# Kernel optimization log

Hardware: AMD Instinct MI355X
Metric: run time of the kernel (lower is better)

## Reference

```python
import jax, jax.numpy as jnp
import numpy as np

N = 50000      # number of nodes (src == dst, homogeneous block)
E = 800000     # number of edges
H = 2          # num_heads
D = 32         # out_dim per head
IN = 64        # target input feature dim
DMID = 64      # 'mid' node-type feature dim
EREL = 200000  # size of 'rel' edge feature table
DREL = 32      # 'rel' edge feature dim
ED = 2 * D     # edge_dim (concat of mid + rel virtual feats per head)


def setup_inputs() -> dict:
    key = jax.random.key(0)
    ks = jax.random.split(key, 18)
    s = 0.05
    return {
        "h": jax.random.normal(ks[0], (N, IN), jnp.float32),
        "W_t": jax.random.normal(ks[1], (IN, H * D), jnp.float32) * s,
        "b_t": jax.random.normal(ks[2], (H * D,), jnp.float32) * s,
        "nfeat_mid": jax.random.normal(ks[3], (N, DMID), jnp.float32),
        "W_mid": jax.random.normal(ks[4], (DMID, H * D), jnp.float32) * s,
        "b_mid": jax.random.normal(ks[5], (H * D,), jnp.float32) * s,
        "efeat_rel": jax.random.normal(ks[6], (EREL, DREL), jnp.float32),
        "W_rel": jax.random.normal(ks[7], (DREL, H * D), jnp.float32) * s,
        "b_rel": jax.random.normal(ks[8], (H * D,), jnp.float32) * s,
        "attn_src": jax.random.normal(ks[9], (1, H, D), jnp.float32) * s,
        "attn_dst": jax.random.normal(ks[10], (1, H, D), jnp.float32) * s,
        "attn_edge": jax.random.normal(ks[11], (1, H, ED), jnp.float32) * s,
        "W_edge": jax.random.normal(ks[12], (ED, D), jnp.float32) * s,
        "b_edge": jax.random.normal(ks[13], (D,), jnp.float32) * s,
        "src_idx": jax.random.randint(ks[14], (E,), 0, N, jnp.int32),
        "dst_idx": jax.random.randint(ks[15], (E,), 0, N, jnp.int32),
        "hn": jax.random.randint(ks[16], (E, 1), 0, N, jnp.int32),
        "he": jax.random.randint(ks[17], (E, 1), 0, EREL, jnp.int32),
    }


def reference(h, W_t, b_t, nfeat_mid, W_mid, b_mid, efeat_rel, W_rel, b_rel,
              attn_src, attn_dst, attn_edge, W_edge, b_edge,
              src_idx, dst_idx, hn, he):
    # target node projection -> [N, H, D]
    hp = (h @ W_t + b_t).reshape(-1, H, D)
    # per-node attention logits (GAT style) -> [N, H]
    e_src = jnp.sum(attn_src * jax.nn.relu(hp), axis=-1)
    e_dst = jnp.sum(attn_dst * jax.nn.relu(hp), axis=-1)
    # per-edge logits: u_add_v -> [E, H]
    e = e_src[src_idx] + e_dst[dst_idx]

    # virtual edge features gathered along metapath: [E, H, 2D]
    hn_f = (nfeat_mid @ W_mid + b_mid).reshape(-1, H, D)[hn[:, 0]]
    he_f = (efeat_rel @ W_rel + b_rel).reshape(-1, H, D)[he[:, 0]]
    h_e = jnp.concatenate([hn_f, he_f], axis=-1)
    e = e + jnp.sum(attn_edge * jax.nn.relu(h_e), axis=-1)

    # edge_softmax: segment softmax over incoming edges of each dst node
    m = jax.ops.segment_max(e, dst_idx, num_segments=N)
    m = jnp.where(jnp.isfinite(m), m, 0.0)  # zero-degree nodes
    ex = jnp.exp(e - m[dst_idx])
    denom = jax.ops.segment_sum(ex, dst_idx, num_segments=N)
    a = ex / denom[dst_idx]                  # [E, H]

    # u_mul_e scatter-sum aggregation -> [N, H, D]
    rst = jax.ops.segment_sum(hp[src_idx] * a[..., None], dst_idx, num_segments=N)
    # edge-feature aggregation -> [N, H, 2D], then fc_edge
    ft2 = jax.ops.segment_sum(h_e * a[..., None], dst_idx, num_segments=N)
    rst = rst + ft2 @ W_edge + b_edge

    # residual + activation
    rst = jax.nn.relu(rst + hp)
    out = rst.reshape(N, H * D)
    # l2 normalize (F.normalize, eps=1e-12)
    out = out / jnp.maximum(jnp.linalg.norm(out, axis=1, keepdims=True), 1e-12)
    return out
```

## Files before the change

### kernel.cpp

```cpp
#include <hip/hip_runtime.h>

typedef unsigned int uint;
#define LOG2E 1.4426950408889634f

__device__ __forceinline__ float bf16_lo(uint v) { return __uint_as_float(v << 16); }
__device__ __forceinline__ float bf16_hi(uint v) { return __uint_as_float(v & 0xffff0000u); }
__device__ __forceinline__ unsigned short f2bf(float f) {
    uint u = __float_as_uint(f);
    return (unsigned short)((u + 0x7fffu + ((u >> 16) & 1u)) >> 16);
}
__device__ __forceinline__ float bf16u(unsigned short s) {
    return __uint_as_float(((uint)s) << 16);
}

template<int K>
__device__ __forceinline__ void proj_body(
    int blk, const float* __restrict__ X, const float* __restrict__ W,
    const float* __restrict__ bias, const float* __restrict__ avec0,
    const float* __restrict__ avec1, int mode, int nrows,
    float* __restrict__ outF32, unsigned short* __restrict__ outF16,
    float2* __restrict__ outA0, float2* __restrict__ outA1,
    float* Xsh, float* Wsh, float* av0sh, float* av1sh, float* bsh)
{
    constexpr int XP = 68;
    int t = threadIdx.x;

    const float4* W4 = (const float4*)W;
    float4* Wsh4 = (float4*)Wsh;
    for (int i = t; i < K * 16; i += 256) Wsh4[i] = W4[i];

    if (t < 64) {
        int head = t >> 5, d = t & 31;
        int aidx = (mode == 0) ? t : (mode == 1 ? head * 64 + d : head * 64 + 32 + d);
        av0sh[t] = avec0 ? avec0[aidx] : 0.f;
        av1sh[t] = avec1 ? avec1[aidx] : 0.f;
        bsh[t] = bias[t];
    }

    int base = blk * 64;
    const float4* X4 = (const float4*)X;
    for (int i = t; i < 64 * (K / 4); i += 256) {
        int row = i / (K / 4), c4 = i % (K / 4);
        int gr = base + row; if (gr >= nrows) gr = nrows - 1;
        *(float4*)&Xsh[row * XP + c4 * 4] = X4[(size_t)gr * (K / 4) + c4];
    }
    __syncthreads();

    int rquad = t >> 4, cq = t & 15;
    float acc[4][4];
#pragma unroll
    for (int ri = 0; ri < 4; ++ri)
#pragma unroll
        for (int ci = 0; ci < 4; ++ci) acc[ri][ci] = 0.f;

#pragma unroll 4
    for (int kq = 0; kq < K / 4; ++kq) {
        float4 wq0 = Wsh4[(4 * kq + 0) * 16 + cq];
        float4 wq1 = Wsh4[(4 * kq + 1) * 16 + cq];
        float4 wq2 = Wsh4[(4 * kq + 2) * 16 + cq];
        float4 wq3 = Wsh4[(4 * kq + 3) * 16 + cq];
#pragma unroll
        for (int ri = 0; ri < 4; ++ri) {
            float4 xq = *(const float4*)&Xsh[(4 * rquad + ri) * XP + 4 * kq];
            acc[ri][0] += xq.x * wq0.x + xq.y * wq1.x + xq.z * wq2.x + xq.w * wq3.x;
            acc[ri][1] += xq.x * wq0.y + xq.y * wq1.y + xq.z * wq2.y + xq.w * wq3.y;
            acc[ri][2] += xq.x * wq0.z + xq.y * wq1.z + xq.z * wq2.z + xq.w * wq3.z;
            acc[ri][3] += xq.x * wq0.w + xq.y * wq1.w + xq.z * wq2.w + xq.w * wq3.w;
        }
    }

    int c0 = cq * 4;
    float4 bv  = *(float4*)&bsh[c0];
    float4 a0v = *(float4*)&av0sh[c0];
    float4 a1v = *(float4*)&av1sh[c0];
    float4 vv[4];
    float s0[4], s1[4];
#pragma unroll
    for (int ri = 0; ri < 4; ++ri) {
        float4 val;
        val.x = acc[ri][0] + bv.x;
        val.y = acc[ri][1] + bv.y;
        val.z = acc[ri][2] + bv.z;
        val.w = acc[ri][3] + bv.w;
        vv[ri] = val;
        float r0 = fmaxf(val.x, 0.f), r1 = fmaxf(val.y, 0.f);
        float r2 = fmaxf(val.z, 0.f), r3 = fmaxf(val.w, 0.f);
        s0[ri] = r0 * a0v.x + r1 * a0v.y + r2 * a0v.z + r3 * a0v.w;
        s1[ri] = r0 * a1v.x + r1 * a1v.y + r2 * a1v.z + r3 * a1v.w;
    }
#pragma unroll
    for (int ri = 0; ri < 4; ++ri) {
        s0[ri] += __shfl_xor(s0[ri], 1, 64);
        s0[ri] += __shfl_xor(s0[ri], 2, 64);
        s0[ri] += __shfl_xor(s0[ri], 4, 64);
        s1[ri] += __shfl_xor(s1[ri], 1, 64);
        s1[ri] += __shfl_xor(s1[ri], 2, 64);
        s1[ri] += __shfl_xor(s1[ri], 4, 64);
    }
    float s0x[4], s1x[4];
#pragma unroll
    for (int ri = 0; ri < 4; ++ri) {
        s0x[ri] = __shfl_xor(s0[ri], 8, 64);
        s1x[ri] = __shfl_xor(s1[ri], 8, 64);
    }

    int rbase = base + rquad * 4;
#pragma unroll
    for (int ri = 0; ri < 4; ++ri) {
        int row = rbase + ri;
        if (row >= nrows) continue;
        if (outF32)
            *(float4*)&outF32[(size_t)row * 64 + c0] = vv[ri];
        uint u0 = (uint)f2bf(vv[ri].x) | ((uint)f2bf(vv[ri].y) << 16);
        uint u1 = (uint)f2bf(vv[ri].z) | ((uint)f2bf(vv[ri].w) << 16);
        *(uint2*)&outF16[(size_t)row * 64 + c0] = make_uint2(u0, u1);
        if (cq == 0 && outA0)
            outA0[row] = make_float2(s0[ri] * LOG2E, s0x[ri] * LOG2E);
        if (cq == 1 && outA1)
            outA1[row] = make_float2(s1[ri] * LOG2E, s1x[ri] * LOG2E);
    }
}

__global__ __launch_bounds__(256) void mega_kernel(
    const float* __restrict__ h, const float* __restrict__ W_t, const float* __restrict__ b_t,
    const float* __restrict__ nfeat_mid, const float* __restrict__ W_mid, const float* __restrict__ b_mid,
    const float* __restrict__ efeat_rel, const float* __restrict__ W_rel, const float* __restrict__ b_rel,
    const float* __restrict__ attn_src, const float* __restrict__ attn_dst, const float* __restrict__ attn_edge,
    const int* __restrict__ dst_idx, int* __restrict__ deg,
    float* __restrict__ hp32, unsigned short* __restrict__ hp16,
    unsigned short* __restrict__ mid16, unsigned short* __restrict__ rel16,
    float2* __restrict__ e_src, float2* __restrict__ e_dst,
    float2* __restrict__ em, float2* __restrict__ er,
    int N, int EREL, int E, int nC, int nA, int nB)
{
    __shared__ float Xsh[64 * 68];
    __shared__ float Wsh[64 * 64];
    __shared__ float av0sh[64], av1sh[64], bsh[64];
    int b = blockIdx.x;
    if (b < nC) {
        proj_body<32>(b, efeat_rel, W_rel, b_rel, attn_edge, nullptr, 2, EREL,
                      nullptr, rel16, er, nullptr, Xsh, Wsh, av0sh, av1sh, bsh);
    } else if (b < nC + nA) {
        proj_body<64>(b - nC, h, W_t, b_t, attn_src, attn_dst, 0, N,
                      hp32, hp16, e_src, e_dst, Xsh, Wsh, av0sh, av1sh, bsh);
    } else if (b < nC + nA + nB) {
        proj_body<64>(b - nC - nA, nfeat_mid, W_mid, b_mid, attn_edge, nullptr, 1, N,
                      nullptr, mid16, em, nullptr, Xsh, Wsh, av0sh, av1sh, bsh);
    } else {
        int i = (b - nC - nA - nB) * 256 + threadIdx.x;
        if (i < E) atomicAdd(&deg[dst_idx[i]], 1);
    }
}

__global__ __launch_bounds__(256) void scanA_kernel(
    const int* __restrict__ deg, int* __restrict__ blkSums, int N)
{
    __shared__ int red[256];
    int t = threadIdx.x;
    int base = blockIdx.x * 1024 + t * 4;
    int s = 0;
    if (base + 3 < N) {
        int4 v = *(const int4*)&deg[base];
        s = v.x + v.y + v.z + v.w;
    } else {
        for (int i = 0; i < 4; ++i) if (base + i < N) s += deg[base + i];
    }
    red[t] = s;
    __syncthreads();
    for (int off = 128; off >= 1; off >>= 1) {
        if (t < off) red[t] += red[t + off];
        __syncthreads();
    }
    if (t == 0) blkSums[blockIdx.x] = red[0];
}

__global__ __launch_bounds__(256) void scanC_kernel(
    const int* __restrict__ deg, const int* __restrict__ blkSums,
    int* __restrict__ row_ptr, int* __restrict__ cursor, int N, int nblk)
{
    __shared__ int sh[256];
    __shared__ int blkOffSh;
    int t = threadIdx.x;
    int blk = blockIdx.x;
    int base = blk * 1024 + t * 4;

    if (t < 64) {
        int s = 0;
        for (int j = t; j < blk; j += 64) s += blkSums[j];
        for (int m = 32; m >= 1; m >>= 1) s += __shfl_xor(s, m, 64);
        if (t == 0) blkOffSh = s;
    }

    int4 v = make_int4(0, 0, 0, 0);
    if (base + 3 < N) v = *(const int4*)&deg[base];
    else {
        if (base < N)     v.x = deg[base];
        if (base + 1 < N) v.y = deg[base + 1];
        if (base + 2 < N) v.z = deg[base + 2];
    }
    int ts = v.x + v.y + v.z + v.w;
    sh[t] = ts;
    __syncthreads();
    for (int off = 1; off < 256; off <<= 1) {
        int val = (t >= off) ? sh[t - off] : 0;
        __syncthreads();
        sh[t] += val;
        __syncthreads();
    }
    int blkOff = blkOffSh;
    int ex = blkOff + ((t == 0) ? 0 : sh[t - 1]);
    int p0 = ex, p1 = ex + v.x, p2 = p1 + v.y, p3 = p2 + v.z;
    if (base < N)     { row_ptr[base]     = p0; cursor[base]     = p0; }
    if (base + 1 < N) { row_ptr[base + 1] = p1; cursor[base + 1] = p1; }
    if (base + 2 < N) { row_ptr[base + 2] = p2; cursor[base + 2] = p2; }
    if (base + 3 < N) { row_ptr[base + 3] = p3; cursor[base + 3] = p3; }
    if (blk == nblk - 1 && t == 255) row_ptr[N] = blkOff + sh[255];
}

__global__ __launch_bounds__(256) void scatter_kernel(
    const int* __restrict__ src, const int* __restrict__ dst,
    const int* __restrict__ hn, const int* __restrict__ he,
    const float2* __restrict__ es, const float2* __restrict__ ed,
    const float2* __restrict__ em, const float2* __restrict__ er,
    int* __restrict__ cursor, uint4* __restrict__ erec, int E)
{
    int i = blockIdx.x * blockDim.x + threadIdx.x;
    if (i >= E) return;
    int s = src[i], d = dst[i], a = hn[i], b = he[i];
    float2 v1 = es[s], v2 = ed[d], v3 = em[a], v4 = er[b];
    float e0 = fminf(fmaxf(v1.x + v2.x + v3.x + v4.x, -60.f), 60.f);
    float e1 = fminf(fmaxf(v1.y + v2.y + v3.y + v4.y, -60.f), 60.f);
    int pos = atomicAdd(&cursor[d], 1);
    erec[pos] = make_uint4((uint)s | ((uint)a << 16), (uint)b,
                           __float_as_uint(e0), __float_as_uint(e1));
}

__global__ __launch_bounds__(256) void aggregate_kernel(
    const int* __restrict__ row_ptr, const uint4* __restrict__ erec,
    const float* __restrict__ hp32,
    const unsigned short* __restrict__ hp16,
    const unsigned short* __restrict__ mid16,
    const unsigned short* __restrict__ rel16,
    const float* __restrict__ We, const float* __restrict__ be,
    float* __restrict__ out, int N)
{
    __shared__ float WeSh[64 * 32];
    __shared__ float ft2sh[4][128];
    int t = threadIdx.x;
    for (int i = t; i < 64 * 32; i += 256) WeSh[i] = We[i];
    __syncthreads();

    int wave = t >> 6, lane = t & 63;
    int head = lane >> 5, dj = lane & 31;
    int n = blockIdx.x * 4 + wave;
    bool valid = n < N;
    int nn = valid ? n : 0;

    int start = row_ptr[nn], end = row_ptr[nn + 1];

    bool isrel = lane >= 32;
    int l31 = lane & 31;
    bool h1w = ((lane >> 4) & 1) != 0;
    const uint* tab32 = (const uint*)(isrel ? rel16 : mid16);
    float rstc = 0.f, fx = 0.f, fy = 0.f, den0 = 0.f, den1 = 0.f;
#pragma unroll 4
    for (int i = start; i < end; ++i) {
        uint4 r = erec[i];
        uint sidx = r.x & 0xffffu;
        float a0 = __builtin_amdgcn_exp2f(__uint_as_float(r.z));
        float a1 = __builtin_amdgcn_exp2f(__uint_as_float(r.w));
        den0 += a0; den1 += a1;
        rstc += bf16u(hp16[(sidx << 6) | (uint)lane]) * (head ? a1 : a0);
        uint ridx = isrel ? r.y : (r.x >> 16);
        uint pv = tab32[(ridx << 5) | (uint)l31];
        float w = h1w ? a1 : a0;
        fx += bf16_lo(pv) * w;
        fy += bf16_hi(pv) * w;
    }
    float inv0 = den0 > 0.f ? 1.f / den0 : 0.f;
    float inv1 = den1 > 0.f ? 1.f / den1 : 0.f;
    rstc *= head ? inv1 : inv0;
    float invf = h1w ? inv1 : inv0;

    int slotbase;
    if (lane < 16)      slotbase = 2 * lane;
    else if (lane < 32) slotbase = 2 * lane + 32;
    else if (lane < 48) slotbase = 2 * lane - 32;
    else                slotbase = 2 * lane;
    ft2sh[wave][slotbase]     = fx * invf;
    ft2sh[wave][slotbase + 1] = fy * invf;

    __builtin_amdgcn_sched_barrier(0);
    asm volatile("s_waitcnt lgkmcnt(0)" ::: "memory");
    __builtin_amdgcn_sched_barrier(0);

    float fc = be[dj];
#pragma unroll 8
    for (int dd = 0; dd < 64; ++dd)
        fc += ft2sh[wave][head * 64 + dd] * WeSh[dd * 32 + dj];

    float val = rstc + fc + hp32[(uint)nn * 64 + lane];
    val = fmaxf(val, 0.f);

    float ss = val * val;
    for (int m = 32; m >= 1; m >>= 1) ss += __shfl_xor(ss, m, 64);
    float invn = 1.f / fmaxf(sqrtf(ss), 1e-12f);
    if (valid) out[(uint)nn * 64 + lane] = val * invn;
}

extern "C" void kernel_launch(void* const* d_in, const int* in_sizes, int n_in,
                              void* d_out, int out_size, void* d_ws, size_t ws_size,
                              hipStream_t stream)
{
    const float* h         = (const float*)d_in[0];
    const float* W_t       = (const float*)d_in[1];
    const float* b_t       = (const float*)d_in[2];
    const float* nfeat_mid = (const float*)d_in[3];
    const float* W_mid     = (const float*)d_in[4];
    const float* b_mid     = (const float*)d_in[5];
    const float* efeat_rel = (const float*)d_in[6];
    const float* W_rel     = (const float*)d_in[7];
    const float* b_rel     = (const float*)d_in[8];
    const float* attn_src  = (const float*)d_in[9];
    const float* attn_dst  = (const float*)d_in[10];
    const float* attn_edge = (const float*)d_in[11];
    const float* W_edge    = (const float*)d_in[12];
    const float* b_edge    = (const float*)d_in[13];
    const int* src_idx     = (const int*)d_in[14];
    const int* dst_idx     = (const int*)d_in[15];
    const int* hn          = (const int*)d_in[16];
    const int* he          = (const int*)d_in[17];
    float* out = (float*)d_out;

    const int N    = in_sizes[0] / 64;
    const int EREL = in_sizes[6] / 32;
    const int E    = in_sizes[14];

    char* ws = (char*)d_ws;
    auto alloc = [&](size_t bytes) {
        void* p = (void*)ws;
        ws += (bytes + 255) & ~(size_t)255;
        return p;
    };
    float* hp32           = (float*)alloc((size_t)N * 64 * 4);
    unsigned short* hp16  = (unsigned short*)alloc((size_t)N * 64 * 2);
    unsigned short* mid16 = (unsigned short*)alloc((size_t)N * 64 * 2);
    unsigned short* rel16 = (unsigned short*)alloc((size_t)EREL * 64 * 2);
    float2* e_src  = (float2*)alloc((size_t)N * 8);
    float2* e_dst  = (float2*)alloc((size_t)N * 8);
    float2* em     = (float2*)alloc((size_t)N * 8);
    float2* er     = (float2*)alloc((size_t)EREL * 8);
    int* deg       = (int*)alloc((size_t)N * 4);
    int* row_ptr   = (int*)alloc((size_t)(N + 1) * 4);
    int* cursor    = (int*)alloc((size_t)N * 4);
    int* blkSums   = (int*)alloc((size_t)64 * 4);
    uint4* erec    = (uint4*)alloc((size_t)E * 16);

    hipMemsetAsync(deg, 0, (size_t)N * 4, stream);

    int nA = (N + 63) / 64;
    int nB = nA;
    int nC = (EREL + 63) / 64;
    int nD = (E + 255) / 256;
    mega_kernel<<<nC + nA + nB + nD, 256, 0, stream>>>(
        h, W_t, b_t, nfeat_mid, W_mid, b_mid, efeat_rel, W_rel, b_rel,
        attn_src, attn_dst, attn_edge, dst_idx, deg,
        hp32, hp16, mid16, rel16, e_src, e_dst, em, er,
        N, EREL, E, nC, nA, nB);

    int nblk = (N + 1023) / 1024;
    scanA_kernel<<<nblk, 256, 0, stream>>>(deg, blkSums, N);
    scanC_kernel<<<nblk, 256, 0, stream>>>(deg, blkSums, row_ptr, cursor, N, nblk);

    scatter_kernel<<<(E + 255) / 256, 256, 0, stream>>>(
        src_idx, dst_idx, hn, he, e_src, e_dst, em, er, cursor, erec, E);

    aggregate_kernel<<<(N + 3) / 4, 256, 0, stream>>>(
        row_ptr, erec, hp32, hp16, mid16, rel16, W_edge, b_edge, out, N);
}
```

Measured before the change: 294.5 us.

## Software-pipeline edge gathers in aggregation and read projection weights from global

The aggregation loop now prefetches the next edge record and its dependent hp16 and table gathers one iteration ahead, so the dependent load chain overlaps with the current edge's arithmetic instead of being serialized. The unroll-by-4 pragma is dropped in favour of this explicit one-deep pipeline. Separately, the projection kernel no longer stages W in shared memory and reads it directly from global/cache, which cuts LDS use (possibly raising occupancy) but adds global loads inside the inner loop.

```diff
diff --git a/kernel.cpp b/kernel.cpp
--- a/kernel.cpp
+++ b/kernel.cpp
@@ -9,8 +9,8 @@
     uint u = __float_as_uint(f);
     return (unsigned short)((u + 0x7fffu + ((u >> 16) & 1u)) >> 16);
 }
-__device__ __forceinline__ float bf16u(unsigned short s) {
-    return __uint_as_float(((uint)s) << 16);
+__device__ __forceinline__ float bf16u(uint s) {
+    return __uint_as_float(s << 16);
 }
 
 template<int K>
@@ -20,14 +20,10 @@
     const float* __restrict__ avec1, int mode, int nrows,
     float* __restrict__ outF32, unsigned short* __restrict__ outF16,
     float2* __restrict__ outA0, float2* __restrict__ outA1,
-    float* Xsh, float* Wsh, float* av0sh, float* av1sh, float* bsh)
+    float* Xsh, float* av0sh, float* av1sh, float* bsh)
 {
     constexpr int XP = 68;
     int t = threadIdx.x;
-
-    const float4* W4 = (const float4*)W;
-    float4* Wsh4 = (float4*)Wsh;
-    for (int i = t; i < K * 16; i += 256) Wsh4[i] = W4[i];
 
     if (t < 64) {
         int head = t >> 5, d = t & 31;
@@ -46,6 +42,7 @@
     }
     __syncthreads();
 
+    const float4* __restrict__ W4 = (const float4*)W;
     int rquad = t >> 4, cq = t & 15;
     float acc[4][4];
 #pragma unroll
@@ -55,10 +52,10 @@
 
 #pragma unroll 4
     for (int kq = 0; kq < K / 4; ++kq) {
-        float4 wq0 = Wsh4[(4 * kq + 0) * 16 + cq];
-        float4 wq1 = Wsh4[(4 * kq + 1) * 16 + cq];
-        float4 wq2 = Wsh4[(4 * kq + 2) * 16 + cq];
-        float4 wq3 = Wsh4[(4 * kq + 3) * 16 + cq];
+        float4 wq0 = W4[(4 * kq + 0) * 16 + cq];
+        float4 wq1 = W4[(4 * kq + 1) * 16 + cq];
+        float4 wq2 = W4[(4 * kq + 2) * 16 + cq];
+        float4 wq3 = W4[(4 * kq + 3) * 16 + cq];
 #pragma unroll
         for (int ri = 0; ri < 4; ++ri) {
             float4 xq = *(const float4*)&Xsh[(4 * rquad + ri) * XP + 4 * kq];
@@ -134,18 +131,17 @@
     int N, int EREL, int E, int nC, int nA, int nB)
 {
     __shared__ float Xsh[64 * 68];
-    __shared__ float Wsh[64 * 64];
     __shared__ float av0sh[64], av1sh[64], bsh[64];
     int b = blockIdx.x;
     if (b < nC) {
         proj_body<32>(b, efeat_rel, W_rel, b_rel, attn_edge, nullptr, 2, EREL,
-                      nullptr, rel16, er, nullptr, Xsh, Wsh, av0sh, av1sh, bsh);
+                      nullptr, rel16, er, nullptr, Xsh, av0sh, av1sh, bsh);
     } else if (b < nC + nA) {
         proj_body<64>(b - nC, h, W_t, b_t, attn_src, attn_dst, 0, N,
-                      hp32, hp16, e_src, e_dst, Xsh, Wsh, av0sh, av1sh, bsh);
+                      hp32, hp16, e_src, e_dst, Xsh, av0sh, av1sh, bsh);
     } else if (b < nC + nA + nB) {
         proj_body<64>(b - nC - nA, nfeat_mid, W_mid, b_mid, attn_edge, nullptr, 1, N,
-                      nullptr, mid16, em, nullptr, Xsh, Wsh, av0sh, av1sh, bsh);
+                      nullptr, mid16, em, nullptr, Xsh, av0sh, av1sh, bsh);
     } else {
         int i = (b - nC - nA - nB) * 256 + threadIdx.x;
         if (i < E) atomicAdd(&deg[dst_idx[i]], 1);
@@ -257,25 +253,37 @@
     int nn = valid ? n : 0;
 
     int start = row_ptr[nn], end = row_ptr[nn + 1];
+    int cnt = end - start;
 
     bool isrel = lane >= 32;
     int l31 = lane & 31;
     bool h1w = ((lane >> 4) & 1) != 0;
     const uint* tab32 = (const uint*)(isrel ? rel16 : mid16);
     float rstc = 0.f, fx = 0.f, fy = 0.f, den0 = 0.f, den1 = 0.f;
-#pragma unroll 4
-    for (int i = start; i < end; ++i) {
-        uint4 r = erec[i];
-        uint sidx = r.x & 0xffffu;
-        float a0 = __builtin_amdgcn_exp2f(__uint_as_float(r.z));
-        float a1 = __builtin_amdgcn_exp2f(__uint_as_float(r.w));
+
+    uint4 rec0 = make_uint4(0, 0, 0, 0);
+    uint hu0 = 0, pv0 = 0;
+    if (cnt > 0) {
+        rec0 = erec[start];
+        hu0 = (uint)hp16[((rec0.x & 0xffffu) << 6) | (uint)lane];
+        pv0 = tab32[((isrel ? rec0.y : (rec0.x >> 16)) << 5) | (uint)l31];
+    }
+    for (int i = 0; i < cnt; ++i) {
+        int j = start + i + 1;
+        int jj = (j < end) ? j : start;
+        uint4 recN = erec[jj];
+        uint huN = (uint)hp16[((recN.x & 0xffffu) << 6) | (uint)lane];
+        uint pvN = tab32[((isrel ? recN.y : (recN.x >> 16)) << 5) | (uint)l31];
+
+        float a0 = __builtin_amdgcn_exp2f(__uint_as_float(rec0.z));
+        float a1 = __builtin_amdgcn_exp2f(__uint_as_float(rec0.w));
         den0 += a0; den1 += a1;
-        rstc += bf16u(hp16[(sidx << 6) | (uint)lane]) * (head ? a1 : a0);
-        uint ridx = isrel ? r.y : (r.x >> 16);
-        uint pv = tab32[(ridx << 5) | (uint)l31];
+        rstc += bf16u(hu0) * (head ? a1 : a0);
         float w = h1w ? a1 : a0;
-        fx += bf16_lo(pv) * w;
-        fy += bf16_hi(pv) * w;
+        fx += bf16_lo(pv0) * w;
+        fy += bf16_hi(pv0) * w;
+
+        rec0 = recN; hu0 = huN; pv0 = pvN;
     }
     float inv0 = den0 > 0.f ? 1.f / den0 : 0.f;
     float inv1 = den1 > 0.f ? 1.f / den1 : 0.f;
```

New measurement: 323.5 us. 1.1x slower.
